# Kernel optimization log

Measured on AMD Instinct MI355X. Metric: run time of the kernel, lower is better.

The kernel has to match this reference:

```python
import jax, jax.numpy as jnp
import numpy as np

B, S, D_IN = 2, 2048, 1024
H = 16
HD = 64  # head_dim = d_out // head_cnt


def setup_inputs() -> dict:
    key = jax.random.key(0)
    kx, kq, kk, kv = jax.random.split(key, 4)
    x = jax.random.normal(kx, (B, S, D_IN), dtype=jnp.float32)
    # Per-head Q/K/V projection weights, stacked: [H, d_in, head_dim].
    # Matches nn.Linear(d_in, head_out) per head (qkv_bias=False), scaled like
    # a typical init.
    sc = 1.0 / np.sqrt(D_IN)
    Wq = jax.random.normal(kq, (H, D_IN, HD), dtype=jnp.float32) * sc
    Wk = jax.random.normal(kk, (H, D_IN, HD), dtype=jnp.float32) * sc
    Wv = jax.random.normal(kv, (H, D_IN, HD), dtype=jnp.float32) * sc
    return {"x": x, "Wq": Wq, "Wk": Wk, "Wv": Wv}


def reference(x, Wq, Wk, Wv):
    # Batched multi-head causal attention equivalent to the per-head loop +
    # torch.cat(dim=-1): head h's output occupies slice [h*HD:(h+1)*HD].
    q = jnp.einsum("bsd,hde->bhse", x, Wq)  # [B,H,S,HD]
    k = jnp.einsum("bsd,hde->bhse", x, Wk)
    v = jnp.einsum("bsd,hde->bhse", x, Wv)
    scale = 1.0 / jnp.sqrt(jnp.asarray(HD, dtype=x.dtype))
    scores = jnp.einsum("bhse,bhte->bhst", q, k) * scale  # [B,H,S,S]
    seq = x.shape[1]
    causal = jnp.tril(jnp.ones((seq, seq), dtype=bool))
    scores = jnp.where(causal, scores, jnp.asarray(-jnp.inf, dtype=scores.dtype))
    attn = jax.nn.softmax(scores, axis=-1)  # dropout = 0.0 -> identity
    ctx = jnp.einsum("bhst,bhte->bhse", attn, v)  # [B,H,S,HD]
    # concat heads on last dim
    b, h, s, e = ctx.shape
    return ctx.transpose(0, 2, 1, 3).reshape(b, s, h * e)
```

## Files before the change

### kernel.cpp

```cpp
#include <hip/hip_runtime.h>


#define DI   1024
#define HD   64
#define NH   16
#define SEQ  2048
#define NB   2

typedef unsigned short u16;
typedef unsigned short us8 __attribute__((ext_vector_type(8)));
typedef unsigned short us4 __attribute__((ext_vector_type(4)));
typedef unsigned int   u32x2 __attribute__((ext_vector_type(2)));
typedef short bf8 __attribute__((ext_vector_type(8)));
typedef float f4 __attribute__((ext_vector_type(4)));

#define MFMA16(a, b, c) __builtin_amdgcn_mfma_f32_16x16x32_bf16((a), (b), (c), 0, 0, 0)

#if __has_builtin(__builtin_amdgcn_exp2f)
#define EXP2(x) __builtin_amdgcn_exp2f(x)
#else
#define EXP2(x) exp2f(x)
#endif

#if __has_builtin(__builtin_amdgcn_perm)
#define PKHI(a, b) __builtin_amdgcn_perm((a), (b), 0x07060302u)
#else
__device__ __forceinline__ unsigned PKHI(unsigned a, unsigned b) {
  return (b >> 16) | (a & 0xffff0000u);
}
#endif

__device__ __forceinline__ u16 f2bf(float f) {
  unsigned u = __float_as_uint(f);
  u += 0x7fffu + ((u >> 16) & 1u);
  return (u16)(u >> 16);
}

__device__ __forceinline__ void async16(const u16* g, u16* l) {
  __builtin_amdgcn_global_load_lds((const __attribute__((address_space(1))) void*)g,
                                   (__attribute__((address_space(3))) void*)l,
                                   16, 0, 0);
}

__global__ __launch_bounds__(256) void prep_k(const float* __restrict__ x,
                                              const float* __restrict__ Wq,
                                              const float* __restrict__ Wk,
                                              const float* __restrict__ Wv,
                                              u16* __restrict__ xb,
                                              u16* __restrict__ Wt) {
  __shared__ __align__(16) u16 tile[64][72];
  const int bid = blockIdx.x;
  if (bid < 2048) {
    const int i = (bid * 256 + threadIdx.x) * 8;
    float4 v0 = *(const float4*)(x + i);
    float4 v1 = *(const float4*)(x + i + 4);
    us8 o;
    o[0] = f2bf(v0.x); o[1] = f2bf(v0.y); o[2] = f2bf(v0.z); o[3] = f2bf(v0.w);
    o[4] = f2bf(v1.x); o[5] = f2bf(v1.y); o[6] = f2bf(v1.z); o[7] = f2bf(v1.w);
    *(us8*)(xb + i) = o;
    return;
  }
  const int idx = bid - 2048;
  const int mh = idx >> 4;
  const int d0 = (idx & 15) * 64;
  const int mat = mh >> 4, h = mh & 15;
  const float* W = (mat == 0 ? Wq : (mat == 1 ? Wk : Wv)) + (size_t)h * DI * HD;
  const int t = threadIdx.x;
  {
    const int r = t >> 2, c = (t & 3) * 16;
    const float* src = W + (size_t)(d0 + r) * HD + c;
    #pragma unroll
    for (int j = 0; j < 4; j++) {
      float4 v = *(const float4*)(src + j * 4);
      tile[r][c + j * 4 + 0] = f2bf(v.x);
      tile[r][c + j * 4 + 1] = f2bf(v.y);
      tile[r][c + j * 4 + 2] = f2bf(v.z);
      tile[r][c + j * 4 + 3] = f2bf(v.w);
    }
  }
  __syncthreads();
  {
    const int e = t >> 2, c = (t & 3) * 16;
    __align__(16) u16 tmp[16];
    #pragma unroll
    for (int i = 0; i < 16; i++) tmp[i] = tile[c + i][e];
    u16* dst = Wt + ((size_t)mh * HD + e) * DI + d0 + c;
    *(us8*)dst       = *(us8*)&tmp[0];
    *(us8*)(dst + 8) = *(us8*)&tmp[8];
  }
}

__global__ __launch_bounds__(256, 2) void proj_k(const u16* __restrict__ x,
                                                 const u16* __restrict__ Wt,
                                                 u16* __restrict__ Qo,
                                                 u16* __restrict__ Ko,
                                                 u16* __restrict__ Vo) {
  __shared__ __align__(16) u16 smem[40960];
  u16* const xs = smem;
  u16* const ws = smem + 16384;
  const int m0 = blockIdx.x * 128, n0 = blockIdx.y * 192;
  const int tid = threadIdx.x, w = tid >> 6, lane = tid & 63;
  const int l15 = lane & 15, quad = lane >> 4, l7 = l15 & 7;
  const int lrow = lane >> 3, lch = lane & 7;
  const int wm = w >> 1, wn = w & 1;

  f4 acc[4][6];
  #pragma unroll
  for (int i = 0; i < 4; i++)
    #pragma unroll
    for (int j = 0; j < 6; j++) {
      f4 z = {0.f, 0.f, 0.f, 0.f};
      acc[i][j] = z;
    }

  const u16* xg = x  + (size_t)(m0 + lrow) * DI + ((lch ^ lrow) * 8);
  const u16* wg = Wt + (size_t)(n0 + lrow) * DI + ((lch ^ lrow) * 8);

  #pragma unroll
  for (int i = 0; i < 4; i++)
    async16(xg + (size_t)(i * 32 + w * 8) * DI, &xs[(i * 32 + w * 8) * 64]);
  #pragma unroll
  for (int c = 0; c < 6; c++)
    async16(wg + (size_t)(w * 48 + c * 8) * DI, &ws[(w * 48 + c * 8) * 64]);

  for (int it = 0; it < 16; it++) {
    const int cbx = (it & 1) * 8192, cbw = (it & 1) * 12288;
    __syncthreads();
    if (it + 1 < 16) {
      const int k1 = (it + 1) * 64;
      const int nbx = 8192 - cbx, nbw = 12288 - cbw;
      #pragma unroll
      for (int i = 0; i < 4; i++)
        async16(xg + (size_t)(i * 32 + w * 8) * DI + k1,
                &xs[nbx + (i * 32 + w * 8) * 64]);
      #pragma unroll
      for (int c = 0; c < 6; c++)
        async16(wg + (size_t)(w * 48 + c * 8) * DI + k1,
                &ws[nbw + (w * 48 + c * 8) * 64]);
    }
    #pragma unroll
    for (int ks = 0; ks < 64; ks += 32) {
      const int c0 = (ks >> 3) + quad;
      bf8 af[4], bfr[6];
      #pragma unroll
      for (int i = 0; i < 4; i++)
        af[i] = *(const bf8*)&xs[cbx + (wm * 64 + i * 16 + l15) * 64 + ((c0 ^ l7) * 8)];
      #pragma unroll
      for (int i = 0; i < 6; i++)
        bfr[i] = *(const bf8*)&ws[cbw + (wn * 96 + i * 16 + l15) * 64 + ((c0 ^ l7) * 8)];
      #pragma unroll
      for (int mi = 0; mi < 4; mi++)
        #pragma unroll
        for (int ni = 0; ni < 6; ni++)
          acc[mi][ni] = MFMA16(af[mi], bfr[ni], acc[mi][ni]);
    }
  }

  const float qscale = 0.125f * 1.44269504088896340736f;
  #pragma unroll
  for (int mi = 0; mi < 4; mi++) {
    const int mrow = m0 + wm * 64 + mi * 16 + quad * 4;
    const int b = mrow >> 11, sb = mrow & (SEQ - 1);
    #pragma unroll
    for (int ni = 0; ni < 6; ni++) {
      const int nf = n0 + wn * 96 + ni * 16;
      const int mat = nf >> 10;
      const int h = (nf >> 6) & 15;
      const int e = (nf & 63) + l15;
      if (mat == 2) {
        __align__(8) u16 pk[4];
        #pragma unroll
        for (int r = 0; r < 4; r++) pk[r] = f2bf(acc[mi][ni][r]);
        *(us4*)(Vo + (((size_t)b * NH + h) * HD + e) * SEQ + sb) = *(us4*)pk;
      } else {
        u16* O = mat ? Ko : Qo;
        const float sc = mat ? 1.0f : qscale;
        #pragma unroll
        for (int r = 0; r < 4; r++)
          O[(((size_t)b * NH + h) * SEQ + sb + r) * HD + e] = f2bf(acc[mi][ni][r] * sc);
      }
    }
  }
}

__global__ __launch_bounds__(256, 2) void attn_k(const u16* __restrict__ Qo,
                                                 const u16* __restrict__ Ko,
                                                 const u16* __restrict__ Vo,
                                                 float* __restrict__ out) {
  __shared__ __align__(16) u16 Ks[2 * 128 * 64];
  __shared__ __align__(16) u16 Vs[2 * 64 * 128];
  __shared__ __align__(16) u16 Ps[4 * 16 * 128];
  const int ia = blockIdx.x;
  const int ib = 31 - ia;
  const int bh = blockIdx.y;
  const int b = bh >> 4, h = bh & 15;
  const int tid = threadIdx.x, w = tid >> 6, lane = tid & 63;
  const int l15 = lane & 15, quad = lane >> 4;
  const int qh = quad >> 1, ql = quad & 1;

  const u16* Qb = Qo + (size_t)bh * SEQ * HD;
  const u16* Kb = Ko + (size_t)bh * SEQ * HD;
  const u16* Vb = Vo + (size_t)bh * HD * SEQ;

  const int qrowA = ia * 64 + w * 16 + l15;
  const int qrowB = ib * 64 + w * 16 + l15;
  bf8 bqA0 = *(const bf8*)(Qb + (size_t)qrowA * HD + quad * 8);
  bf8 bqA1 = *(const bf8*)(Qb + (size_t)qrowA * HD + 32 + quad * 8);
  bf8 bqB0 = *(const bf8*)(Qb + (size_t)qrowB * HD + quad * 8);
  bf8 bqB1 = *(const bf8*)(Qb + (size_t)qrowB * HD + 32 + quad * 8);

  f4 oA[4], oB[4], lA, lB;
  #pragma unroll
  for (int i = 0; i < 4; i++) {
    f4 z = {0.f, 0.f, 0.f, 0.f};
    oA[i] = z; oB[i] = z;
  }
  {
    f4 z = {0.f, 0.f, 0.f, 0.f};
    lA = z; lB = z;
  }
  const bf8 ones = {0x3F80, 0x3F80, 0x3F80, 0x3F80, 0x3F80, 0x3F80, 0x3F80, 0x3F80};

  const int nA = ia / 2 + 1, nB = ib / 2 + 1;

  const u16* ksp0 = &Ks[l15 * 64 + ((quad ^ (l15 & 7)) * 8)];
  const u16* ksp1 = &Ks[l15 * 64 + (((quad + 4) ^ (l15 & 7)) * 8)];
  const u16* vsp[4];
  #pragma unroll
  for (int tc = 0; tc < 4; tc++)
    vsp[tc] = &Vs[l15 * 128 + (((tc * 4 + quad) ^ l15) * 8)];
  u16* const psw = &Ps[w * 2048 + l15 * 128 + ql * 4];
  const u16* prp[4];
  #pragma unroll
  for (int tc = 0; tc < 4; tc++)
    prp[tc] = &Ps[w * 2048 + l15 * 128 + (((tc * 4 + quad) ^ l15) * 8)];

  const int kl = lane >> 3, kc = lane & 7;
  const int vl = lane >> 4, vc = lane & 15;
  const u16* kg = Kb + (size_t)(w * 32 + kl) * HD + ((kc ^ kl) * 8);
  const u16* vg[4];
  u16* ldsK[4];
  u16* ldsV[4];
  #pragma unroll
  for (int i = 0; i < 4; i++) {
    const int vr = w * 16 + i * 4;
    const int f = (i * 4 + vl) & 15;
    vg[i] = Vb + (size_t)(vr + vl) * SEQ + ((vc ^ f) * 8);
    ldsK[i] = &Ks[(w * 32 + i * 8) * 64];
    ldsV[i] = &Vs[vr * 128];
  }

  const int mqA = qrowA - (nA - 1) * 128 - quad * 4;
  const int mqB = qrowB - (nB - 1) * 128 - quad * 4;

  auto pphase = [&](f4* s, bool domask, int mq) {
    #pragma unroll
    for (int mf = 0; mf < 8; mf++) {
      f4 sv = s[mf];
      if (domask) {
        #pragma unroll
        for (int r = 0; r < 4; r++)
          sv[r] = (mf * 16 + r <= mq) ? sv[r] : -1e30f;
      }
      const unsigned p0 = __float_as_uint(EXP2(sv[0]));
      const unsigned p1 = __float_as_uint(EXP2(sv[1]));
      const unsigned p2 = __float_as_uint(EXP2(sv[2]));
      const unsigned p3 = __float_as_uint(EXP2(sv[3]));
      u32x2 pk = {PKHI(p1, p0), PKHI(p3, p2)};
      *(u32x2*)(psw + ((((mf << 1) | qh) ^ l15) * 8)) = pk;
    }
  };

  #pragma unroll
  for (int i = 0; i < 4; i++) {
    async16(kg + i * 512, ldsK[i]);
    async16(vg[i], ldsV[i]);
  }
  kg += 128 * HD;
  #pragma unroll
  for (int i = 0; i < 4; i++) vg[i] += 128;

  for (int it = 0; it < nB; it++) {
    const int cb = (it & 1) * 8192;
    __syncthreads();
    if (it + 1 < nB) {
      const int nb = 8192 - cb;
      #pragma unroll
      for (int i = 0; i < 4; i++) {
        async16(kg + i * 512, ldsK[i] + nb);
        async16(vg[i], ldsV[i] + nb);
      }
      kg += 128 * HD;
      #pragma unroll
      for (int i = 0; i < 4; i++) vg[i] += 128;
    }
    const bool doA = (it < nA);

    f4 sA[8], sB[8];
    #pragma unroll
    for (int mf = 0; mf < 8; mf++) {
      bf8 ak0 = *(const bf8*)(ksp0 + cb + mf * 1024);
      bf8 ak1 = *(const bf8*)(ksp1 + cb + mf * 1024);
      f4 z = {0.f, 0.f, 0.f, 0.f};
      f4 tb = MFMA16(ak0, bqB0, z);
      sB[mf] = MFMA16(ak1, bqB1, tb);
      if (doA) {
        f4 ta = MFMA16(ak0, bqA0, z);
        sA[mf] = MFMA16(ak1, bqA1, ta);
      }
    }

    pphase(sB, it == nB - 1, mqB);
    #pragma unroll
    for (int tc = 0; tc < 4; tc++) {
      bf8 pf = *(const bf8*)(prp[tc]);
      lB = MFMA16(ones, pf, lB);
      #pragma unroll
      for (int ef = 0; ef < 4; ef++) {
        bf8 vf = *(const bf8*)(vsp[tc] + cb + ef * 2048);
        oB[ef] = MFMA16(vf, pf, oB[ef]);
      }
    }
    if (doA) {
      pphase(sA, it == nA - 1, mqA);
      #pragma unroll
      for (int tc = 0; tc < 4; tc++) {
        bf8 pf = *(const bf8*)(prp[tc]);
        lA = MFMA16(ones, pf, lA);
        #pragma unroll
        for (int ef = 0; ef < 4; ef++) {
          bf8 vf = *(const bf8*)(vsp[tc] + cb + ef * 2048);
          oA[ef] = MFMA16(vf, pf, oA[ef]);
        }
      }
    }
  }

  const float invA = 1.0f / lA[0];
  const float invB = 1.0f / lB[0];
  float* opA = out + ((size_t)b * SEQ + qrowA) * (NH * HD) + h * HD + quad * 4;
  float* opB = out + ((size_t)b * SEQ + qrowB) * (NH * HD) + h * HD + quad * 4;
  #pragma unroll
  for (int ef = 0; ef < 4; ef++) {
    f4 va = oA[ef] * invA;
    f4 vb = oB[ef] * invB;
    *(float4*)(opA + ef * 16) = *(float4*)&va;
    *(float4*)(opB + ef * 16) = *(float4*)&vb;
  }
}

extern "C" void kernel_launch(void* const* d_in, const int* in_sizes, int n_in,
                              void* d_out, int out_size, void* d_ws, size_t ws_size,
                              hipStream_t stream) {
  const float* x  = (const float*)d_in[0];
  const float* Wq = (const float*)d_in[1];
  const float* Wk = (const float*)d_in[2];
  const float* Wv = (const float*)d_in[3];
  float* out = (float*)d_out;

  u16* xb = (u16*)d_ws;
  u16* Wt = xb + (size_t)NB * SEQ * DI;
  u16* Qo = Wt + (size_t)3 * NH * HD * DI;
  u16* Ko = Qo + (size_t)NB * NH * SEQ * HD;
  u16* Vo = Ko + (size_t)NB * NH * SEQ * HD;

  prep_k<<<dim3(2048 + 768), 256, 0, stream>>>(x, Wq, Wk, Wv, xb, Wt);
  proj_k<<<dim3(32, 16), 256, 0, stream>>>(xb, Wt, Qo, Ko, Vo);
  attn_k<<<dim3(16, 32), 256, 0, stream>>>(Qo, Ko, Vo, out);
}
```

Baseline: 143.8 us.

## Replace paired causal q-tiles with one q-tile per block and 64-wide KV tiles

The attention kernel drops the scheme where each block handled two mirrored 64-row query tiles (ia and 31-ia) over shared 128-wide KV tiles. Each block now owns one query tile and walks 64-wide K/V tiles, launching twice as many blocks, heaviest tiles first, with halved shared memory and launch bounds raised to 4 blocks per CU. This aims for more occupancy and simpler per-iteration work, at the cost of losing K/V reuse across two query tiles, more LDS loads per MFMA, more barriers per unit of work, and relying on reverse launch order rather than pairing for load balance.

```diff
diff --git a/kernel.cpp b/kernel.cpp
--- a/kernel.cpp
+++ b/kernel.cpp
@@ -183,79 +183,94 @@
   }
 }
 
-__global__ __launch_bounds__(256, 2) void attn_k(const u16* __restrict__ Qo,
+__global__ __launch_bounds__(256, 4) void attn_k(const u16* __restrict__ Qo,
                                                  const u16* __restrict__ Ko,
                                                  const u16* __restrict__ Vo,
                                                  float* __restrict__ out) {
-  __shared__ __align__(16) u16 Ks[2 * 128 * 64];
-  __shared__ __align__(16) u16 Vs[2 * 64 * 128];
-  __shared__ __align__(16) u16 Ps[4 * 16 * 128];
-  const int ia = blockIdx.x;
-  const int ib = 31 - ia;
+  __shared__ __align__(16) u16 Ks[2 * 64 * 64];
+  __shared__ __align__(16) u16 Vs[2 * 64 * 64];
+  __shared__ __align__(16) u16 Ps[4 * 16 * 64];
+  const int qt = 31 - (int)blockIdx.x;
   const int bh = blockIdx.y;
   const int b = bh >> 4, h = bh & 15;
   const int tid = threadIdx.x, w = tid >> 6, lane = tid & 63;
-  const int l15 = lane & 15, quad = lane >> 4;
+  const int l15 = lane & 15, quad = lane >> 4, l7 = l15 & 7;
   const int qh = quad >> 1, ql = quad & 1;
 
   const u16* Qb = Qo + (size_t)bh * SEQ * HD;
   const u16* Kb = Ko + (size_t)bh * SEQ * HD;
   const u16* Vb = Vo + (size_t)bh * HD * SEQ;
 
-  const int qrowA = ia * 64 + w * 16 + l15;
-  const int qrowB = ib * 64 + w * 16 + l15;
-  bf8 bqA0 = *(const bf8*)(Qb + (size_t)qrowA * HD + quad * 8);
-  bf8 bqA1 = *(const bf8*)(Qb + (size_t)qrowA * HD + 32 + quad * 8);
-  bf8 bqB0 = *(const bf8*)(Qb + (size_t)qrowB * HD + quad * 8);
-  bf8 bqB1 = *(const bf8*)(Qb + (size_t)qrowB * HD + 32 + quad * 8);
-
-  f4 oA[4], oB[4], lA, lB;
+  const int qrow = qt * 64 + w * 16 + l15;
+  bf8 bq0 = *(const bf8*)(Qb + (size_t)qrow * HD + quad * 8);
+  bf8 bq1 = *(const bf8*)(Qb + (size_t)qrow * HD + 32 + quad * 8);
+
+  f4 oacc[4], lacc;
   #pragma unroll
   for (int i = 0; i < 4; i++) {
     f4 z = {0.f, 0.f, 0.f, 0.f};
-    oA[i] = z; oB[i] = z;
+    oacc[i] = z;
   }
   {
     f4 z = {0.f, 0.f, 0.f, 0.f};
-    lA = z; lB = z;
+    lacc = z;
   }
   const bf8 ones = {0x3F80, 0x3F80, 0x3F80, 0x3F80, 0x3F80, 0x3F80, 0x3F80, 0x3F80};
 
-  const int nA = ia / 2 + 1, nB = ib / 2 + 1;
-
-  const u16* ksp0 = &Ks[l15 * 64 + ((quad ^ (l15 & 7)) * 8)];
-  const u16* ksp1 = &Ks[l15 * 64 + (((quad + 4) ^ (l15 & 7)) * 8)];
-  const u16* vsp[4];
-  #pragma unroll
-  for (int tc = 0; tc < 4; tc++)
-    vsp[tc] = &Vs[l15 * 128 + (((tc * 4 + quad) ^ l15) * 8)];
-  u16* const psw = &Ps[w * 2048 + l15 * 128 + ql * 4];
-  const u16* prp[4];
-  #pragma unroll
-  for (int tc = 0; tc < 4; tc++)
-    prp[tc] = &Ps[w * 2048 + l15 * 128 + (((tc * 4 + quad) ^ l15) * 8)];
+  const int niter = qt + 1;
+
+  const u16* ksp0 = &Ks[l15 * 64 + ((quad ^ l7) * 8)];
+  const u16* ksp1 = &Ks[l15 * 64 + (((quad + 4) ^ l7) * 8)];
+  const u16* vsp[2];
+  #pragma unroll
+  for (int tc = 0; tc < 2; tc++)
+    vsp[tc] = &Vs[l15 * 64 + (((tc * 4 + quad) ^ l7) * 8)];
+  u16* const psw = &Ps[w * 1024 + l15 * 64 + ql * 4];
+  const u16* prp[2];
+  #pragma unroll
+  for (int tc = 0; tc < 2; tc++)
+    prp[tc] = &Ps[w * 1024 + l15 * 64 + (((tc * 4 + quad) ^ l7) * 8)];
 
   const int kl = lane >> 3, kc = lane & 7;
-  const int vl = lane >> 4, vc = lane & 15;
-  const u16* kg = Kb + (size_t)(w * 32 + kl) * HD + ((kc ^ kl) * 8);
-  const u16* vg[4];
-  u16* ldsK[4];
-  u16* ldsV[4];
-  #pragma unroll
-  for (int i = 0; i < 4; i++) {
-    const int vr = w * 16 + i * 4;
-    const int f = (i * 4 + vl) & 15;
-    vg[i] = Vb + (size_t)(vr + vl) * SEQ + ((vc ^ f) * 8);
-    ldsK[i] = &Ks[(w * 32 + i * 8) * 64];
-    ldsV[i] = &Vs[vr * 128];
-  }
-
-  const int mqA = qrowA - (nA - 1) * 128 - quad * 4;
-  const int mqB = qrowB - (nB - 1) * 128 - quad * 4;
-
-  auto pphase = [&](f4* s, bool domask, int mq) {
-    #pragma unroll
-    for (int mf = 0; mf < 8; mf++) {
+  const int sw = (kc ^ kl) * 8;
+  const u16* kg = Kb + (size_t)(w * 16 + kl) * HD + sw;
+  const u16* vg = Vb + (size_t)(w * 16 + kl) * SEQ + sw;
+  u16* const ldsK = &Ks[(w * 16) * 64];
+  u16* const ldsV = &Vs[(w * 16) * 64];
+
+  const int mq = qrow - qt * 64 - quad * 4;
+
+  async16(kg, ldsK);
+  async16(kg + 8 * HD, ldsK + 512);
+  async16(vg, ldsV);
+  async16(vg + 8 * SEQ, ldsV + 512);
+  kg += 64 * HD; vg += 64;
+
+  for (int it = 0; it < niter; it++) {
+    const int cb = (it & 1) * 4096;
+    __syncthreads();
+    if (it + 1 < niter) {
+      const int nb = 4096 - cb;
+      async16(kg, ldsK + nb);
+      async16(kg + 8 * HD, ldsK + nb + 512);
+      async16(vg, ldsV + nb);
+      async16(vg + 8 * SEQ, ldsV + nb + 512);
+      kg += 64 * HD; vg += 64;
+    }
+
+    f4 s[4];
+    #pragma unroll
+    for (int mf = 0; mf < 4; mf++) {
+      bf8 ak0 = *(const bf8*)(ksp0 + cb + mf * 1024);
+      bf8 ak1 = *(const bf8*)(ksp1 + cb + mf * 1024);
+      f4 z = {0.f, 0.f, 0.f, 0.f};
+      f4 t = MFMA16(ak0, bq0, z);
+      s[mf] = MFMA16(ak1, bq1, t);
+    }
+
+    const bool domask = (it == niter - 1);
+    #pragma unroll
+    for (int mf = 0; mf < 4; mf++) {
       f4 sv = s[mf];
       if (domask) {
         #pragma unroll
@@ -267,85 +282,27 @@
       const unsigned p2 = __float_as_uint(EXP2(sv[2]));
       const unsigned p3 = __float_as_uint(EXP2(sv[3]));
       u32x2 pk = {PKHI(p1, p0), PKHI(p3, p2)};
-      *(u32x2*)(psw + ((((mf << 1) | qh) ^ l15) * 8)) = pk;
-    }
-  };
-
-  #pragma unroll
-  for (int i = 0; i < 4; i++) {
-    async16(kg + i * 512, ldsK[i]);
-    async16(vg[i], ldsV[i]);
-  }
-  kg += 128 * HD;
-  #pragma unroll
-  for (int i = 0; i < 4; i++) vg[i] += 128;
-
-  for (int it = 0; it < nB; it++) {
-    const int cb = (it & 1) * 8192;
-    __syncthreads();
-    if (it + 1 < nB) {
-      const int nb = 8192 - cb;
-      #pragma unroll
-      for (int i = 0; i < 4; i++) {
-        async16(kg + i * 512, ldsK[i] + nb);
-        async16(vg[i], ldsV[i] + nb);
+      *(u32x2*)(psw + (((mf * 2 + qh) ^ l7) * 8)) = pk;
+    }
+
+    #pragma unroll
+    for (int tc = 0; tc < 2; tc++) {
+      bf8 pf = *(const bf8*)(prp[tc]);
+      lacc = MFMA16(ones, pf, lacc);
+      #pragma unroll
+      for (int ef = 0; ef < 4; ef++) {
+        bf8 vf = *(const bf8*)(vsp[tc] + cb + ef * 1024);
+        oacc[ef] = MFMA16(vf, pf, oacc[ef]);
       }
-      kg += 128 * HD;
-      #pragma unroll
-      for (int i = 0; i < 4; i++) vg[i] += 128;
-    }
-    const bool doA = (it < nA);
-
-    f4 sA[8], sB[8];
-    #pragma unroll
-    for (int mf = 0; mf < 8; mf++) {
-      bf8 ak0 = *(const bf8*)(ksp0 + cb + mf * 1024);
-      bf8 ak1 = *(const bf8*)(ksp1 + cb + mf * 1024);
-      f4 z = {0.f, 0.f, 0.f, 0.f};
-      f4 tb = MFMA16(ak0, bqB0, z);
-      sB[mf] = MFMA16(ak1, bqB1, tb);
-      if (doA) {
-        f4 ta = MFMA16(ak0, bqA0, z);
-        sA[mf] = MFMA16(ak1, bqA1, ta);
-      }
-    }
-
-    pphase(sB, it == nB - 1, mqB);
-    #pragma unroll
-    for (int tc = 0; tc < 4; tc++) {
-      bf8 pf = *(const bf8*)(prp[tc]);
-      lB = MFMA16(ones, pf, lB);
-      #pragma unroll
-      for (int ef = 0; ef < 4; ef++) {
-        bf8 vf = *(const bf8*)(vsp[tc] + cb + ef * 2048);
-        oB[ef] = MFMA16(vf, pf, oB[ef]);
-      }
-    }
-    if (doA) {
-      pphase(sA, it == nA - 1, mqA);
-      #pragma unroll
-      for (int tc = 0; tc < 4; tc++) {
-        bf8 pf = *(const bf8*)(prp[tc]);
-        lA = MFMA16(ones, pf, lA);
-        #pragma unroll
-        for (int ef = 0; ef < 4; ef++) {
-          bf8 vf = *(const bf8*)(vsp[tc] + cb + ef * 2048);
-          oA[ef] = MFMA16(vf, pf, oA[ef]);
-        }
-      }
-    }
-  }
-
-  const float invA = 1.0f / lA[0];
-  const float invB = 1.0f / lB[0];
-  float* opA = out + ((size_t)b * SEQ + qrowA) * (NH * HD) + h * HD + quad * 4;
-  float* opB = out + ((size_t)b * SEQ + qrowB) * (NH * HD) + h * HD + quad * 4;
+    }
+  }
+
+  const float inv = 1.0f / lacc[0];
+  float* op = out + ((size_t)b * SEQ + qrow) * (NH * HD) + h * HD + quad * 4;
   #pragma unroll
   for (int ef = 0; ef < 4; ef++) {
-    f4 va = oA[ef] * invA;
-    f4 vb = oB[ef] * invB;
-    *(float4*)(opA + ef * 16) = *(float4*)&va;
-    *(float4*)(opB + ef * 16) = *(float4*)&vb;
+    f4 v = oacc[ef] * inv;
+    *(float4*)(op + ef * 16) = *(float4*)&v;
   }
 }
 
@@ -366,5 +323,5 @@
 
   prep_k<<<dim3(2048 + 768), 256, 0, stream>>>(x, Wq, Wk, Wv, xb, Wt);
   proj_k<<<dim3(32, 16), 256, 0, stream>>>(xb, Wt, Qo, Ko, Vo);
-  attn_k<<<dim3(16, 32), 256, 0, stream>>>(Qo, Ko, Vo, out);
-}
+  attn_k<<<dim3(32, 32), 256, 0, stream>>>(Qo, Ko, Vo, out);
+}
```

Result: slower. 155.4 us (+8.1%).
